# Kernel tuning notes

Hardware: AMD Instinct MI355X
Metric: run time of the kernel (lower is better)

The kernel has to match this reference:

```python
import jax, jax.numpy as jnp
import numpy as np

B, S, D = 2, 2048, 1024
H = 16
DH = D // H  # 64

def setup_inputs() -> dict:
    key = jax.random.key(0)
    ks = jax.random.split(key, 7)
    sc = 1.0 / np.sqrt(DH)
    return {
        "sequences": jax.random.normal(ks[0], (B, S, D), dtype=jnp.float32),
        "Wq": jax.random.normal(ks[1], (H, DH, DH), dtype=jnp.float32) * sc,
        "bq": jax.random.normal(ks[2], (H, DH), dtype=jnp.float32) * 0.02,
        "Wk": jax.random.normal(ks[3], (H, DH, DH), dtype=jnp.float32) * sc,
        "bk": jax.random.normal(ks[4], (H, DH), dtype=jnp.float32) * 0.02,
        "Wv": jax.random.normal(ks[5], (H, DH, DH), dtype=jnp.float32) * sc,
        "bv": jax.random.normal(ks[6], (H, DH), dtype=jnp.float32) * 0.02,
    }

def reference(sequences, Wq, bq, Wk, bk, Wv, bv):
    b, s, _ = sequences.shape
    x = sequences.reshape(b, s, H, DH)  # [B,S,H,Dh]
    # torch Linear: y = x @ W^T + b; W is [out,in] => einsum contracts input dim d
    q = jnp.einsum("bshd,hed->bshe", x, Wq) + bq  # [B,S,H,Dh]
    k = jnp.einsum("bshd,hed->bshe", x, Wk) + bk
    v = jnp.einsum("bshd,hed->bshe", x, Wv) + bv
    scores = jnp.einsum("bshd,bthd->bhst", q, k) / jnp.sqrt(jnp.float32(DH))
    attn = jax.nn.softmax(scores, axis=-1)  # [B,H,S,S]
    out = jnp.einsum("bhst,bthd->bshd", attn, v)  # [B,S,H,Dh]
    return out.reshape(b, s, H * DH)
```

## Files before the change

### kernel.cpp

```cpp
#include <hip/hip_runtime.h>

typedef unsigned short u16;
typedef __bf16 bf16x8 __attribute__((ext_vector_type(8)));
typedef float  f32x4  __attribute__((ext_vector_type(4)));
typedef u16    u16x4  __attribute__((ext_vector_type(4)));

#define HH   16
#define DHH  64
#define SEQL 2048
#define NB   2
#define BHN  (NB * HH)

static __device__ __forceinline__ u16 f2bf(float f) {
    return __builtin_bit_cast(u16, (__bf16)f);
}

static __device__ __forceinline__ void gload_lds16(const void* g, void* l) {
    __builtin_amdgcn_global_load_lds(
        (const __attribute__((address_space(1))) unsigned int*)g,
        (__attribute__((address_space(3))) unsigned int*)l, 16, 0, 0);
}

__global__ __launch_bounds__(256) void qkv_kernel(
    const float* __restrict__ x,
    const float* __restrict__ Wq, const float* __restrict__ bq,
    const float* __restrict__ Wk, const float* __restrict__ bk,
    const float* __restrict__ Wv, const float* __restrict__ bv,
    u16* __restrict__ Qws, u16* __restrict__ Kws, u16* __restrict__ Vtws)
{
    const int h   = blockIdx.y;
    const int r0  = blockIdx.x * 64;
    const int tid = threadIdx.x;
    const int w   = tid >> 6;
    const int l   = tid & 63;
    const int c   = l & 15;
    const int g   = l >> 4;

    __shared__ u16 vt[64 * 72];

    bf16x8 xa[2];
    {
        const float* xp = x + (size_t)(r0 + w * 16 + c) * 1024 + h * 64 + g * 8;
        #pragma unroll
        for (int kh = 0; kh < 2; ++kh) {
            float4 lo = *reinterpret_cast<const float4*>(xp + kh * 32);
            float4 hi = *reinterpret_cast<const float4*>(xp + kh * 32 + 4);
            bf16x8 f;
            f[0]=(__bf16)lo.x; f[1]=(__bf16)lo.y; f[2]=(__bf16)lo.z; f[3]=(__bf16)lo.w;
            f[4]=(__bf16)hi.x; f[5]=(__bf16)hi.y; f[6]=(__bf16)hi.z; f[7]=(__bf16)hi.w;
            xa[kh] = f;
        }
    }

    const int b      = r0 >> 11;
    const int s_base = r0 & (SEQL - 1);
    const int bh     = b * HH + h;

    const float* Ws[3] = {Wq + h * 64 * 64, Wk + h * 64 * 64, Wv + h * 64 * 64};
    const float* bs[3] = {bq + h * 64,      bk + h * 64,      bv + h * 64};

    #pragma unroll
    for (int m = 0; m < 3; ++m) {
        const float* W    = Ws[m];
        const float* bias = bs[m];
        f32x4 acc[4];
        #pragma unroll
        for (int ct = 0; ct < 4; ++ct) {
            acc[ct][0] = 0.f; acc[ct][1] = 0.f; acc[ct][2] = 0.f; acc[ct][3] = 0.f;
        }
        #pragma unroll
        for (int kh = 0; kh < 2; ++kh) {
            #pragma unroll
            for (int ct = 0; ct < 4; ++ct) {
                const float* wp = W + (ct * 16 + c) * 64 + kh * 32 + g * 8;
                float4 lo = *reinterpret_cast<const float4*>(wp);
                float4 hi = *reinterpret_cast<const float4*>(wp + 4);
                bf16x8 wf;
                wf[0]=(__bf16)lo.x; wf[1]=(__bf16)lo.y; wf[2]=(__bf16)lo.z; wf[3]=(__bf16)lo.w;
                wf[4]=(__bf16)hi.x; wf[5]=(__bf16)hi.y; wf[6]=(__bf16)hi.z; wf[7]=(__bf16)hi.w;
                acc[ct] = __builtin_amdgcn_mfma_f32_16x16x32_bf16(xa[kh], wf, acc[ct], 0, 0, 0);
            }
        }
        if (m < 2) {
            u16* outp = (m == 0 ? Qws : Kws) +
                        ((size_t)bh * SEQL + s_base + w * 16 + g * 4) * 64;
            #pragma unroll
            for (int ct = 0; ct < 4; ++ct) {
                float bb = bias[ct * 16 + c];
                #pragma unroll
                for (int r = 0; r < 4; ++r)
                    outp[(size_t)r * 64 + ct * 16 + c] = f2bf(acc[ct][r] + bb);
            }
        } else {
            #pragma unroll
            for (int ct = 0; ct < 4; ++ct) {
                float bb = bias[ct * 16 + c];
                #pragma unroll
                for (int r = 0; r < 4; ++r)
                    vt[(ct * 16 + c) * 72 + w * 16 + g * 4 + r] = f2bf(acc[ct][r] + bb);
            }
        }
    }
    __syncthreads();
    {
        const int d  = tid >> 2;
        const int s0 = (tid & 3) * 16;
        u16* vp = Vtws + ((size_t)bh * 64 + d) * SEQL + s_base + s0;
        uint4 v0 = *reinterpret_cast<const uint4*>(&vt[d * 72 + s0]);
        uint4 v1 = *reinterpret_cast<const uint4*>(&vt[d * 72 + s0 + 8]);
        *reinterpret_cast<uint4*>(vp)     = v0;
        *reinterpret_cast<uint4*>(vp + 8) = v1;
    }
}

__global__ __launch_bounds__(256) void attn_kernel(
    const u16* __restrict__ Qws, const u16* __restrict__ Kws,
    const u16* __restrict__ Vtws, float* __restrict__ out)
{
    const int p     = blockIdx.x;
    const int lid   = (p & 7) * 64 + (p >> 3);
    const int qtile = lid & 15;
    const int bh    = lid >> 4;
    const int b     = bh >> 4;
    const int h     = bh & 15;

    const int tid = threadIdx.x;
    const int w   = tid >> 6;
    const int l   = tid & 63;
    const int c   = l & 15;
    const int g   = l >> 4;
    const int q0  = qtile * 128 + w * 32;

    __shared__ u16 k_lds[2][64 * 64];
    __shared__ u16 v_lds[2][64 * 64];
    __shared__ u16 plds_all[4 * 32 * 64];
    char* pbase = reinterpret_cast<char*>(plds_all + w * (32 * 64));

    const u16* Kb = Kws  + (size_t)bh * SEQL * 64;
    const u16* Vb = Vtws + (size_t)bh * 64 * SEQL;

    const int rs8 = l >> 3;
    const int sx  = (l & 7) ^ rs8;

    #define STAGE(bb, k0)                                                     \
    {   _Pragma("unroll")                                                     \
        for (int a = 0; a < 2; ++a) {                                         \
            const int rbase = w * 16 + a * 8;                                 \
            const int r     = rbase + rs8;                                    \
            gload_lds16(Kb + (size_t)((k0) + r) * 64 + sx * 8,                \
                        &k_lds[bb][rbase * 64]);                              \
            gload_lds16(Vb + (size_t)r * SEQL + (k0) + sx * 8,                \
                        &v_lds[bb][rbase * 64]);                              \
        }                                                                     \
    }

    bf16x8 qf[2][2];
    #pragma unroll
    for (int qt = 0; qt < 2; ++qt)
        #pragma unroll
        for (int kh = 0; kh < 2; ++kh)
            qf[qt][kh] = *reinterpret_cast<const bf16x8*>(
                Qws + ((size_t)bh * SEQL + q0 + qt * 16 + c) * 64 + kh * 32 + g * 8);

    f32x4 acc[4][2];
    #pragma unroll
    for (int dt = 0; dt < 4; ++dt)
        #pragma unroll
        for (int qt = 0; qt < 2; ++qt) {
            acc[dt][qt][0]=0.f; acc[dt][qt][1]=0.f; acc[dt][qt][2]=0.f; acc[dt][qt][3]=0.f;
        }
    float mrow[2] = {-1e30f, -1e30f};
    float lrow[2] = {0.f, 0.f};
    const float SCL = 0.125f * 1.44269504088896340736f;

    const int rdoff = ((g ^ (c & 7)) * 8);

    STAGE(0, 0);
    __syncthreads();

    for (int t = 0; t < SEQL / 64; ++t) {
        const int cur = t & 1;

        if (t + 1 < SEQL / 64) STAGE(cur ^ 1, (t + 1) * 64);

        f32x4 st[4][2];
        #pragma unroll
        for (int kt = 0; kt < 4; ++kt)
            #pragma unroll
            for (int qt = 0; qt < 2; ++qt) {
                st[kt][qt][0]=0.f; st[kt][qt][1]=0.f; st[kt][qt][2]=0.f; st[kt][qt][3]=0.f;
            }
        #pragma unroll
        for (int kt = 0; kt < 4; ++kt) {
            const int e0 = (kt * 16 + c) * 64 + rdoff;
            bf16x8 ka0 = *reinterpret_cast<const bf16x8*>(&k_lds[cur][e0]);
            bf16x8 ka1 = *reinterpret_cast<const bf16x8*>(&k_lds[cur][e0 ^ 32]);
            #pragma unroll
            for (int qt = 0; qt < 2; ++qt) {
                st[kt][qt] = __builtin_amdgcn_mfma_f32_16x16x32_bf16(ka0, qf[qt][0], st[kt][qt], 0, 0, 0);
                st[kt][qt] = __builtin_amdgcn_mfma_f32_16x16x32_bf16(ka1, qf[qt][1], st[kt][qt], 0, 0, 0);
            }
        }

        bf16x8 vf[8];
        #pragma unroll
        for (int dt = 0; dt < 4; ++dt) {
            const int e0 = (dt * 16 + c) * 64 + rdoff;
            vf[dt * 2]     = *reinterpret_cast<const bf16x8*>(&v_lds[cur][e0]);
            vf[dt * 2 + 1] = *reinterpret_cast<const bf16x8*>(&v_lds[cur][e0 ^ 32]);
        }

        #pragma unroll
        for (int qt = 0; qt < 2; ++qt) {
            float mx = st[0][qt][0];
            #pragma unroll
            for (int kt = 0; kt < 4; ++kt)
                #pragma unroll
                for (int r = 0; r < 4; ++r)
                    mx = fmaxf(mx, st[kt][qt][r]);
            mx = fmaxf(mx, __shfl_xor(mx, 16, 64));
            mx = fmaxf(mx, __shfl_xor(mx, 32, 64));
            const float mx_s = mx * SCL;

            if (!__all(mx_s <= mrow[qt] + 8.f)) {
                const float mn    = fmaxf(mrow[qt], mx_s);
                const float alpha = __builtin_amdgcn_exp2f(mrow[qt] - mn);
                mrow[qt] = mn;
                lrow[qt] *= alpha;
                #pragma unroll
                for (int dt = 0; dt < 4; ++dt) {
                    acc[dt][qt][0] *= alpha; acc[dt][qt][1] *= alpha;
                    acc[dt][qt][2] *= alpha; acc[dt][qt][3] *= alpha;
                }
            }

            float rs = 0.f;
            const int row = qt * 16 + c;
            #pragma unroll
            for (int kt = 0; kt < 4; ++kt) {
                u16x4 pb;
                #pragma unroll
                for (int r = 0; r < 4; ++r) {
                    float pv = __builtin_amdgcn_exp2f(fmaf(st[kt][qt][r], SCL, -mrow[qt]));
                    rs += pv;
                    pb[r] = f2bf(pv);
                }
                const int blk = (kt * 2 + (g >> 1)) ^ (row & 7);
                *reinterpret_cast<u16x4*>(pbase + row * 128 + blk * 16 + (g & 1) * 8) = pb;
            }
            rs += __shfl_xor(rs, 16, 64);
            rs += __shfl_xor(rs, 32, 64);
            lrow[qt] += rs;
        }

        asm volatile("s_waitcnt lgkmcnt(0)" ::: "memory");

        bf16x8 pf[2][2];
        #pragma unroll
        for (int qt = 0; qt < 2; ++qt) {
            const int row = qt * 16 + c;
            #pragma unroll
            for (int kh = 0; kh < 2; ++kh) {
                const int blk = (kh * 4 + g) ^ (row & 7);
                pf[qt][kh] = *reinterpret_cast<const bf16x8*>(pbase + row * 128 + blk * 16);
            }
        }

        #pragma unroll
        for (int dt = 0; dt < 4; ++dt) {
            #pragma unroll
            for (int qt = 0; qt < 2; ++qt) {
                acc[dt][qt] = __builtin_amdgcn_mfma_f32_16x16x32_bf16(vf[dt*2],   pf[qt][0], acc[dt][qt], 0, 0, 0);
                acc[dt][qt] = __builtin_amdgcn_mfma_f32_16x16x32_bf16(vf[dt*2+1], pf[qt][1], acc[dt][qt], 0, 0, 0);
            }
        }

        __syncthreads();
    }

    const float inv0 = 1.f / lrow[0];
    const float inv1 = 1.f / lrow[1];
    #pragma unroll
    for (int qt = 0; qt < 2; ++qt) {
        const float inv = qt ? inv1 : inv0;
        float* op = out + ((size_t)b * SEQL + q0 + qt * 16 + c) * 1024 + h * 64 + g * 4;
        #pragma unroll
        for (int dt = 0; dt < 4; ++dt) {
            float4 o;
            o.x = acc[dt][qt][0] * inv; o.y = acc[dt][qt][1] * inv;
            o.z = acc[dt][qt][2] * inv; o.w = acc[dt][qt][3] * inv;
            *reinterpret_cast<float4*>(op + dt * 16) = o;
        }
    }
}

extern "C" void kernel_launch(void* const* d_in, const int* in_sizes, int n_in,
                              void* d_out, int out_size, void* d_ws, size_t ws_size,
                              hipStream_t stream) {
    const float* x  = (const float*)d_in[0];
    const float* Wq = (const float*)d_in[1];
    const float* bq = (const float*)d_in[2];
    const float* Wk = (const float*)d_in[3];
    const float* bk = (const float*)d_in[4];
    const float* Wv = (const float*)d_in[5];
    const float* bv = (const float*)d_in[6];
    float* out = (float*)d_out;

    const size_t per = (size_t)BHN * SEQL * 64;
    u16* Qws = (u16*)d_ws;
    u16* Kws = Qws + per;
    u16* Vt  = Kws + per;

    qkv_kernel<<<dim3(64, 16), 256, 0, stream>>>(x, Wq, bq, Wk, bk, Wv, bv, Qws, Kws, Vt);
    attn_kernel<<<dim3(512), 256, 0, stream>>>(Qws, Kws, Vt, out);
}
```

Measured before the change: 95.41 us.

## Prepack weights to bf16, compute softmax row sums with MFMA, add setprio

```diff
diff --git a/kernel.cpp b/kernel.cpp
--- a/kernel.cpp
+++ b/kernel.cpp
@@ -21,11 +21,22 @@
         (__attribute__((address_space(3))) unsigned int*)l, 16, 0, 0);
 }
 
+__global__ __launch_bounds__(256) void wconv_kernel(
+    const float* __restrict__ Wq, const float* __restrict__ Wk,
+    const float* __restrict__ Wv, u16* __restrict__ Wb)
+{
+    const int m = blockIdx.y;
+    const float* W = (m == 0) ? Wq : (m == 1) ? Wk : Wv;
+    const int i = (blockIdx.x * 256 + threadIdx.x) * 4;
+    float4 v = *reinterpret_cast<const float4*>(W + i);
+    u16x4 o = { f2bf(v.x), f2bf(v.y), f2bf(v.z), f2bf(v.w) };
+    *reinterpret_cast<u16x4*>(Wb + (size_t)m * 65536 + i) = o;
+}
+
 __global__ __launch_bounds__(256) void qkv_kernel(
-    const float* __restrict__ x,
-    const float* __restrict__ Wq, const float* __restrict__ bq,
-    const float* __restrict__ Wk, const float* __restrict__ bk,
-    const float* __restrict__ Wv, const float* __restrict__ bv,
+    const float* __restrict__ x, const u16* __restrict__ Wb,
+    const float* __restrict__ bq, const float* __restrict__ bk,
+    const float* __restrict__ bv,
     u16* __restrict__ Qws, u16* __restrict__ Kws, u16* __restrict__ Vtws)
 {
     const int h   = blockIdx.y;
@@ -56,12 +67,11 @@
     const int s_base = r0 & (SEQL - 1);
     const int bh     = b * HH + h;
 
-    const float* Ws[3] = {Wq + h * 64 * 64, Wk + h * 64 * 64, Wv + h * 64 * 64};
-    const float* bs[3] = {bq + h * 64,      bk + h * 64,      bv + h * 64};
+    const float* bs[3] = {bq + h * 64, bk + h * 64, bv + h * 64};
 
     #pragma unroll
     for (int m = 0; m < 3; ++m) {
-        const float* W    = Ws[m];
+        const u16*   W    = Wb + (size_t)m * 65536 + h * 4096;
         const float* bias = bs[m];
         f32x4 acc[4];
         #pragma unroll
@@ -72,12 +82,8 @@
         for (int kh = 0; kh < 2; ++kh) {
             #pragma unroll
             for (int ct = 0; ct < 4; ++ct) {
-                const float* wp = W + (ct * 16 + c) * 64 + kh * 32 + g * 8;
-                float4 lo = *reinterpret_cast<const float4*>(wp);
-                float4 hi = *reinterpret_cast<const float4*>(wp + 4);
-                bf16x8 wf;
-                wf[0]=(__bf16)lo.x; wf[1]=(__bf16)lo.y; wf[2]=(__bf16)lo.z; wf[3]=(__bf16)lo.w;
-                wf[4]=(__bf16)hi.x; wf[5]=(__bf16)hi.y; wf[6]=(__bf16)hi.z; wf[7]=(__bf16)hi.w;
+                bf16x8 wf = *reinterpret_cast<const bf16x8*>(
+                    W + (ct * 16 + c) * 64 + kh * 32 + g * 8);
                 acc[ct] = __builtin_amdgcn_mfma_f32_16x16x32_bf16(xa[kh], wf, acc[ct], 0, 0, 0);
             }
         }
@@ -95,9 +101,11 @@
             #pragma unroll
             for (int ct = 0; ct < 4; ++ct) {
                 float bb = bias[ct * 16 + c];
+                u16x4 pb;
                 #pragma unroll
                 for (int r = 0; r < 4; ++r)
-                    vt[(ct * 16 + c) * 72 + w * 16 + g * 4 + r] = f2bf(acc[ct][r] + bb);
+                    pb[r] = f2bf(acc[ct][r] + bb);
+                *reinterpret_cast<u16x4*>(&vt[(ct * 16 + c) * 72 + w * 16 + g * 4]) = pb;
             }
         }
     }
@@ -162,13 +170,16 @@
             qf[qt][kh] = *reinterpret_cast<const bf16x8*>(
                 Qws + ((size_t)bh * SEQL + q0 + qt * 16 + c) * 64 + kh * 32 + g * 8);
 
+    const f32x4 zero4 = {0.f, 0.f, 0.f, 0.f};
+    bf16x8 ones8;
+    #pragma unroll
+    for (int j = 0; j < 8; ++j) ones8[j] = __builtin_bit_cast(__bf16, (u16)0x3F80);
+
     f32x4 acc[4][2];
     #pragma unroll
     for (int dt = 0; dt < 4; ++dt)
         #pragma unroll
-        for (int qt = 0; qt < 2; ++qt) {
-            acc[dt][qt][0]=0.f; acc[dt][qt][1]=0.f; acc[dt][qt][2]=0.f; acc[dt][qt][3]=0.f;
-        }
+        for (int qt = 0; qt < 2; ++qt) acc[dt][qt] = zero4;
     float mrow[2] = {-1e30f, -1e30f};
     float lrow[2] = {0.f, 0.f};
     const float SCL = 0.125f * 1.44269504088896340736f;
@@ -184,12 +195,7 @@
         if (t + 1 < SEQL / 64) STAGE(cur ^ 1, (t + 1) * 64);
 
         f32x4 st[4][2];
-        #pragma unroll
-        for (int kt = 0; kt < 4; ++kt)
-            #pragma unroll
-            for (int qt = 0; qt < 2; ++qt) {
-                st[kt][qt][0]=0.f; st[kt][qt][1]=0.f; st[kt][qt][2]=0.f; st[kt][qt][3]=0.f;
-            }
+        __builtin_amdgcn_s_setprio(1);
         #pragma unroll
         for (int kt = 0; kt < 4; ++kt) {
             const int e0 = (kt * 16 + c) * 64 + rdoff;
@@ -197,10 +203,11 @@
             bf16x8 ka1 = *reinterpret_cast<const bf16x8*>(&k_lds[cur][e0 ^ 32]);
             #pragma unroll
             for (int qt = 0; qt < 2; ++qt) {
-                st[kt][qt] = __builtin_amdgcn_mfma_f32_16x16x32_bf16(ka0, qf[qt][0], st[kt][qt], 0, 0, 0);
+                st[kt][qt] = __builtin_amdgcn_mfma_f32_16x16x32_bf16(ka0, qf[qt][0], zero4,      0, 0, 0);
                 st[kt][qt] = __builtin_amdgcn_mfma_f32_16x16x32_bf16(ka1, qf[qt][1], st[kt][qt], 0, 0, 0);
             }
         }
+        __builtin_amdgcn_s_setprio(0);
 
         bf16x8 vf[8];
         #pragma unroll
@@ -212,12 +219,17 @@
 
         #pragma unroll
         for (int qt = 0; qt < 2; ++qt) {
-            float mx = st[0][qt][0];
-            #pragma unroll
-            for (int kt = 0; kt < 4; ++kt)
-                #pragma unroll
-                for (int r = 0; r < 4; ++r)
-                    mx = fmaxf(mx, st[kt][qt][r]);
+            float a0 = fmaxf(st[0][qt][0], st[0][qt][1]);
+            float a1 = fmaxf(st[0][qt][2], st[0][qt][3]);
+            float a2 = fmaxf(st[1][qt][0], st[1][qt][1]);
+            float a3 = fmaxf(st[1][qt][2], st[1][qt][3]);
+            float a4 = fmaxf(st[2][qt][0], st[2][qt][1]);
+            float a5 = fmaxf(st[2][qt][2], st[2][qt][3]);
+            float a6 = fmaxf(st[3][qt][0], st[3][qt][1]);
+            float a7 = fmaxf(st[3][qt][2], st[3][qt][3]);
+            float b0 = fmaxf(fmaxf(a0, a1), fmaxf(a2, a3));
+            float b1 = fmaxf(fmaxf(a4, a5), fmaxf(a6, a7));
+            float mx = fmaxf(b0, b1);
             mx = fmaxf(mx, __shfl_xor(mx, 16, 64));
             mx = fmaxf(mx, __shfl_xor(mx, 32, 64));
             const float mx_s = mx * SCL;
@@ -234,23 +246,16 @@
                 }
             }
 
-            float rs = 0.f;
             const int row = qt * 16 + c;
             #pragma unroll
             for (int kt = 0; kt < 4; ++kt) {
                 u16x4 pb;
                 #pragma unroll
-                for (int r = 0; r < 4; ++r) {
-                    float pv = __builtin_amdgcn_exp2f(fmaf(st[kt][qt][r], SCL, -mrow[qt]));
-                    rs += pv;
-                    pb[r] = f2bf(pv);
-                }
+                for (int r = 0; r < 4; ++r)
+                    pb[r] = f2bf(__builtin_amdgcn_exp2f(fmaf(st[kt][qt][r], SCL, -mrow[qt])));
                 const int blk = (kt * 2 + (g >> 1)) ^ (row & 7);
                 *reinterpret_cast<u16x4*>(pbase + row * 128 + blk * 16 + (g & 1) * 8) = pb;
             }
-            rs += __shfl_xor(rs, 16, 64);
-            rs += __shfl_xor(rs, 32, 64);
-            lrow[qt] += rs;
         }
 
         asm volatile("s_waitcnt lgkmcnt(0)" ::: "memory");
@@ -266,6 +271,7 @@
             }
         }
 
+        __builtin_amdgcn_s_setprio(1);
         #pragma unroll
         for (int dt = 0; dt < 4; ++dt) {
             #pragma unroll
@@ -274,6 +280,15 @@
                 acc[dt][qt] = __builtin_amdgcn_mfma_f32_16x16x32_bf16(vf[dt*2+1], pf[qt][1], acc[dt][qt], 0, 0, 0);
             }
         }
+        f32x4 su[2];
+        #pragma unroll
+        for (int qt = 0; qt < 2; ++qt) {
+            su[qt] = __builtin_amdgcn_mfma_f32_16x16x32_bf16(ones8, pf[qt][0], zero4,   0, 0, 0);
+            su[qt] = __builtin_amdgcn_mfma_f32_16x16x32_bf16(ones8, pf[qt][1], su[qt], 0, 0, 0);
+        }
+        __builtin_amdgcn_s_setprio(0);
+        lrow[0] += su[0][0];
+        lrow[1] += su[1][0];
 
         __syncthreads();
     }
@@ -310,7 +325,9 @@
     u16* Qws = (u16*)d_ws;
     u16* Kws = Qws + per;
     u16* Vt  = Kws + per;
-
-    qkv_kernel<<<dim3(64, 16), 256, 0, stream>>>(x, Wq, bq, Wk, bk, Wv, bv, Qws, Kws, Vt);
+    u16* Wb  = Vt  + per;
+
+    wconv_kernel<<<dim3(64, 3), 256, 0, stream>>>(Wq, Wk, Wv, Wb);
+    qkv_kernel<<<dim3(64, 16), 256, 0, stream>>>(x, Wb, bq, bk, bv, Qws, Kws, Vt);
     attn_kernel<<<dim3(512), 256, 0, stream>>>(Qws, Kws, Vt, out);
 }
```

New measurement: 89.23 us. 1.07x faster.
